# Kernel optimization log

Hardware: AMD Instinct MI355X
Metric: run time of the kernel (lower is better)

The kernel has to match this reference:

```python
import jax, jax.numpy as jnp
import numpy as np

HEADS, DIM, N = 16, 128, 2048
NEG = -1e9


def setup_inputs() -> dict:
    key = jax.random.key(0)
    ks = jax.random.split(key, 8)
    xavier = lambda k, shape, fan: jax.random.uniform(
        k, shape, jnp.float32, -1.0, 1.0) * np.sqrt(6.0 / fan)
    return {
        "q": jax.random.normal(ks[0], (N, DIM), jnp.float32),
        "k": jax.random.normal(ks[1], (N, DIM), jnp.float32),
        "v": jax.random.normal(ks[2], (N, DIM), jnp.float32),
        "mask": jax.random.randint(ks[3], (N, N), 0, 2) > 0,
        "Q": xavier(ks[4], (HEADS, DIM, DIM), 2 * DIM),
        "K": xavier(ks[5], (HEADS, DIM, DIM), 2 * DIM),
        "V": xavier(ks[6], (HEADS, DIM, DIM), 2 * DIM),
        "last": xavier(ks[7], (HEADS * DIM, DIM), HEADS * DIM + DIM),
    }


def reference(q, k, v, Q, K, V, last, mask):
    # per-head projections: [n, d] x [h, d, d] -> [h, n, d]
    qp = jnp.einsum('nd,hde->hne', q, Q)
    kp = jnp.einsum('nd,hde->hne', k, K)
    vp = jnp.einsum('nd,hde->hne', v, V)
    n = qp.shape[1]
    # NOTE: original computes k @ q^T and scales by sqrt(seq_len) (q.size(1) after projection)
    att = jnp.einsum('hid,hjd->hij', kp, qp)  # [h, n, n]
    fmask = mask.astype(jnp.float32)
    att = att * fmask / jnp.sqrt(jnp.float32(n)) + NEG * (1.0 - fmask)
    att = jax.nn.softmax(att, axis=2)
    out = jnp.einsum('hij,hjd->hid', att, vp)            # [h, n, d]
    out = jnp.transpose(out, (1, 0, 2)).reshape(n, -1)   # n (heads d)
    return out @ last
```

## Files before the change

### kernel.cpp

```cpp
#include <hip/hip_runtime.h>
#include <hip/hip_bf16.h>


#define HN 16
#define NN 2048
#define DD 128

typedef __attribute__((ext_vector_type(8))) short short8;
typedef __attribute__((ext_vector_type(4))) short short4v;
typedef __attribute__((ext_vector_type(4))) float float4v;
typedef __attribute__((ext_vector_type(16))) float f32x16;
typedef __attribute__((ext_vector_type(4))) unsigned int uint4v;

#define CROW(r) ((((r) & 3)) + 8 * ((r) >> 2))

__device__ inline unsigned short f2bf(float f) {
    unsigned int u = __builtin_bit_cast(unsigned int, f);
    unsigned int r = (u + 0x7fffu + ((u >> 16) & 1u)) >> 16;
    return (unsigned short)r;
}

__device__ inline unsigned int cvtpk(float lo, float hi) {
    unsigned int w;
    asm("v_cvt_pk_bf16_f32 %0, %1, %2" : "=v"(w) : "v"(lo), "v"(hi));
    return w;
}

__device__ inline void plswap(unsigned int& x, unsigned int& y) {
#if __has_builtin(__builtin_amdgcn_permlane32_swap)
    typedef int int2v __attribute__((ext_vector_type(2)));
    int2v r = __builtin_amdgcn_permlane32_swap((int)x, (int)y, false, false);
    x = (unsigned int)r[0];
    y = (unsigned int)r[1];
#else
    const unsigned int sx = (unsigned int)__shfl_xor((int)x, 32);
    const unsigned int sy = (unsigned int)__shfl_xor((int)y, 32);
    const bool hiHalf = (threadIdx.x & 32) != 0;
    const unsigned int nx = hiHalf ? sy : x;
    const unsigned int ny = hiHalf ? y : sx;
    x = nx; y = ny;
#endif
}

__device__ inline void bar_lds() {
    asm volatile("s_waitcnt lgkmcnt(0)" ::: "memory");
    __builtin_amdgcn_sched_barrier(0);
    __builtin_amdgcn_s_barrier();
    __builtin_amdgcn_sched_barrier(0);
}

__device__ inline short8 ld_bf8(const float* __restrict__ p) {
    const float4v a = *(const float4v*)p;
    const float4v b = *(const float4v*)(p + 4);
    short8 r;
    r[0] = (short)f2bf(a[0]); r[1] = (short)f2bf(a[1]);
    r[2] = (short)f2bf(a[2]); r[3] = (short)f2bf(a[3]);
    r[4] = (short)f2bf(b[0]); r[5] = (short)f2bf(b[1]);
    r[6] = (short)f2bf(b[2]); r[7] = (short)f2bf(b[3]);
    return r;
}

__device__ inline short8 ld2x4(const unsigned short* p) {
    const short4v lo = *(const short4v*)p;
    const short4v hi = *(const short4v*)(p + 4);
    short8 r;
    r[0] = lo[0]; r[1] = lo[1]; r[2] = lo[2]; r[3] = lo[3];
    r[4] = hi[0]; r[5] = hi[1]; r[6] = hi[2]; r[7] = hi[3];
    return r;
}

__global__ void sentinel_kernel(float* out, int n) {
    int i = blockIdx.x * 256 + threadIdx.x;
    if (i < n) out[i] = 2.0f;
}

__global__ __launch_bounds__(256) void maskpack2_kernel(
    const int* __restrict__ mask,
    unsigned long long* __restrict__ mb,
    float* __restrict__ out, int out_n)
{
    const int wgrp = blockIdx.x * 4 + (threadIdx.x >> 6);
    const int lane = threadIdx.x & 63;
    const int word0 = wgrp * 4;
    const int i = word0 >> 5;
    const int w = word0 & 31;
    const int* row = mask + (size_t)i * NN + w * 64;
    unsigned long long b[4];
#pragma unroll
    for (int c = 0; c < 4; c++)
        b[c] = __ballot(row[c * 64 + lane] != 0);
    if (lane == 0) {
#pragma unroll
        for (int c = 0; c < 4; c++) mb[word0 + c] = b[c];
    }
    const int z = blockIdx.x * 256 + threadIdx.x;
    if (z < out_n) out[z] = 0.f;
}

__global__ __launch_bounds__(256) void wprep_kernel(
    const float* __restrict__ Qw,
    const float* __restrict__ Kw,
    const float* __restrict__ Vw,
    unsigned short* __restrict__ wsW)
{
    __shared__ __align__(16) unsigned short Wt[128 * 132];
    const int h = blockIdx.x, t = blockIdx.y;
    const float* W = ((t == 0) ? Qw : ((t == 1) ? Kw : Vw)) + h * DD * DD;
    unsigned short* o = wsW + ((size_t)t * HN + h) * DD * DD;
    const int tid = threadIdx.x;

    for (int idx2 = tid * 2; idx2 < DD * DD; idx2 += 512) {
        const int d = idx2 >> 7, e = idx2 & 127;
        const float2 w2 = *(const float2*)(W + idx2);
        Wt[(e + 0) * 132 + d] = f2bf(w2.x);
        Wt[(e + 1) * 132 + d] = f2bf(w2.y);
    }
    __syncthreads();
    for (int idx8 = tid * 8; idx8 < DD * DD; idx8 += 2048) {
        const int e = idx8 >> 7, d = idx8 & 127;
        *(short8*)(o + idx8) = ld2x4(&Wt[e * 132 + d]);
    }
}

__global__ __launch_bounds__(256) void proj3_kernel(
    const float* __restrict__ q,
    const float* __restrict__ k,
    const float* __restrict__ v,
    const unsigned short* __restrict__ wsW,
    unsigned short* __restrict__ ws)
{
    __shared__ __align__(16) unsigned short Wt[128 * 136];
    const int t = blockIdx.z, h = blockIdx.y, cb = blockIdx.x;
    const int tid = threadIdx.x;
    const float* in = (t == 0) ? q : ((t == 1) ? k : v);
    const unsigned short* WTg = wsW + ((size_t)t * HN + h) * DD * DD;
    unsigned short* out = ws + (size_t)t * (HN * NN * DD) + (size_t)h * (NN * DD);

#pragma unroll
    for (int it = 0; it < 8; it++) {
        const int idx8 = tid * 8 + it * 2048;
        const int row = idx8 >> 7, col = idx8 & 127;
        *(short8*)(&Wt[row * 136 + col]) = *(const short8*)(WTg + idx8);
    }
    __syncthreads();

    const int wave = tid >> 6, lane = tid & 63;
    const int quad = lane >> 4, l16 = lane & 15;

#pragma unroll 1
    for (int rt = 0; rt < 2; rt++) {
        const int row0 = cb * 128 + rt * 64 + wave * 16;

        float4v acc[8];
#pragma unroll
        for (int c = 0; c < 8; c++) acc[c] = {0.f, 0.f, 0.f, 0.f};

        if (t < 2) {
#pragma unroll
            for (int kk = 0; kk < 4; kk++) {
                const short8 a = ld_bf8(in + (size_t)(row0 + l16) * DD + kk * 32 + quad * 8);
#pragma unroll
                for (int c = 0; c < 8; c++) {
                    const short8 b = *(const short8*)(&Wt[(c * 16 + l16) * 136 + kk * 32 + quad * 8]);
                    acc[c] = __builtin_amdgcn_mfma_f32_16x16x32_bf16(a, b, acc[c], 0, 0, 0);
                }
            }
#pragma unroll
            for (int c = 0; c < 8; c++)
#pragma unroll
                for (int r = 0; r < 4; r++)
                    out[(size_t)(row0 + quad * 4 + r) * DD + c * 16 + l16] = f2bf(acc[c][r]);
        } else {
#pragma unroll
            for (int kk = 0; kk < 4; kk++) {
                const short8 bv = ld_bf8(in + (size_t)(row0 + l16) * DD + kk * 32 + quad * 8);
#pragma unroll
                for (int c = 0; c < 8; c++) {
                    const short8 aw = *(const short8*)(&Wt[(c * 16 + l16) * 136 + kk * 32 + quad * 8]);
                    acc[c] = __builtin_amdgcn_mfma_f32_16x16x32_bf16(aw, bv, acc[c], 0, 0, 0);
                }
            }
#pragma unroll
            for (int c = 0; c < 8; c++)
#pragma unroll
                for (int r = 0; r < 4; r++)
                    out[(size_t)(c * 16 + quad * 4 + r) * NN + row0 + l16] = f2bf(acc[c][r]);
        }
    }
}

__global__ __launch_bounds__(256, 2) void attn_kernel(
    unsigned short* __restrict__ ws,
    const unsigned long long* __restrict__ mb)
{
    __shared__ __align__(16) unsigned short qs[2][64 * 136];
    __shared__ __align__(16) unsigned short vpTile[2][128 * 72];

    const int h = blockIdx.y, ib = blockIdx.x;
    const int tid = threadIdx.x;
    const int wave = tid >> 6, lane = tid & 63;
    const int ig = wave >> 1;
    const int h2 = wave & 1;
    const int l31 = lane & 31;
    const int hi = lane >> 5;

    const unsigned short* qp  = ws + (size_t)h * (NN * DD);
    const unsigned short* kp  = ws + (size_t)(HN * NN * DD) + (size_t)h * (NN * DD);
    const unsigned short* vpT = ws + (size_t)(2 * HN * NN * DD) + (size_t)h * (NN * DD);
    unsigned short* ao = ws + (size_t)(3 * HN * NN * DD);

    const int i0 = ib * 64;
    const float scale = 0.022097086912079612f;

    short8 kpf[8];
    {
        const int row = i0 + ig * 32 + l31;
#pragma unroll
        for (int kk = 0; kk < 8; kk++)
            kpf[kk] = *(const short8*)(kp + (size_t)row * DD + kk * 16 + hi * 8);
    }

    short8 rq[4], rv[4];

#define LOADT(J0) do {                                                         \
        _Pragma("unroll")                                                      \
        for (int it = 0; it < 4; it++) {                                       \
            const int idx = tid * 8 + it * 2048;                               \
            rq[it] = *(const short8*)(qp + (size_t)(J0) * DD + idx);           \
            rv[it] = *(const short8*)(vpT + (size_t)(idx >> 6) * NN + (J0) + (idx & 63)); \
        } } while (0)

#define WRITET(BUF) do {                                                       \
        _Pragma("unroll")                                                      \
        for (int it = 0; it < 4; it++) {                                       \
            const int idx = tid * 8 + it * 2048;                               \
            *(short8*)(&qs[BUF][(idx >> 7) * 136 + (idx & 127)]) = rq[it];     \
            *(short8*)(&vpTile[BUF][(idx >> 6) * 72 + (idx & 63)]) = rv[it];   \
        } } while (0)

    f32x16 o[4];
#pragma unroll
    for (int dt = 0; dt < 4; dt++)
#pragma unroll
        for (int r = 0; r < 16; r++) o[dt][r] = 0.f;
    float lacc = 0.f;

    auto COMPUTE = [&](int buf, int jt) {
        const unsigned long long mrow = mb[(size_t)(i0 + ig * 32 + l31) * 32 + jt];
        const unsigned int m2 = (unsigned int)(mrow >> (h2 * 32 + hi * 4));

        f32x16 s;
#pragma unroll
        for (int r = 0; r < 16; r++) s[r] = 0.f;
        __builtin_amdgcn_s_setprio(1);
#pragma unroll
        for (int kk = 0; kk < 8; kk++) {
            const short8 aq = *(const short8*)(&qs[buf][(h2 * 32 + l31) * 136 + kk * 16 + hi * 8]);
            s = __builtin_amdgcn_mfma_f32_32x32x16_bf16(aq, kpf[kk], s, 0, 0, 0);
        }
        __builtin_amdgcn_s_setprio(0);

#pragma unroll
        for (int r = 0; r < 16; r++) {
            const float x = ((m2 >> CROW(r)) & 1u) ? fmaf(s[r], scale, -5.0f) : -50.0f;
            s[r] = __expf(x);
        }
        float ls = (((s[0] + s[1]) + (s[2] + s[3])) + ((s[4] + s[5]) + (s[6] + s[7])))
                 + (((s[8] + s[9]) + (s[10] + s[11])) + ((s[12] + s[13]) + (s[14] + s[15])));
        ls += __shfl_xor(ls, 32);
        lacc += ls;

        short8 pa[2];
#pragma unroll
        for (int ks = 0; ks < 2; ks++) {
            const int b = ks * 8;
            unsigned int x0 = cvtpk(s[b + 0], s[b + 1]);
            unsigned int y0 = cvtpk(s[b + 4], s[b + 5]);
            unsigned int x1 = cvtpk(s[b + 2], s[b + 3]);
            unsigned int y1 = cvtpk(s[b + 6], s[b + 7]);
            plswap(x0, y0);
            plswap(x1, y1);
            uint4v w; w[0] = x0; w[1] = x1; w[2] = y0; w[3] = y1;
            pa[ks] = __builtin_bit_cast(short8, w);
        }

        __builtin_amdgcn_s_setprio(1);
#pragma unroll
        for (int ks = 0; ks < 2; ks++) {
#pragma unroll
            for (int dt = 0; dt < 4; dt++) {
                const short8 bv = *(const short8*)(&vpTile[buf][(dt * 32 + l31) * 72 + h2 * 32 + ks * 16 + hi * 8]);
                o[dt] = __builtin_amdgcn_mfma_f32_32x32x16_bf16(pa[ks], bv, o[dt], 0, 0, 0);
            }
        }
        __builtin_amdgcn_s_setprio(0);
    };

    LOADT(0);
    WRITET(0);
    LOADT(64);
    __syncthreads();

    int cur = 0;

#pragma unroll 1
    for (int jt = 0; jt < 30; ++jt) {
        WRITET(cur ^ 1);
        LOADT((jt + 2) * 64);
        COMPUTE(cur, jt);
        bar_lds();
        cur ^= 1;
    }
    WRITET(cur ^ 1);
    COMPUTE(cur, 30);
    bar_lds();
    cur ^= 1;
    COMPUTE(cur, 31);

#undef LOADT
#undef WRITET

    __syncthreads();
    float* obuf = (float*)&qs[0][0];
    float* lbuf = (float*)&vpTile[0][0];

    if (h2 == 1) {
#pragma unroll
        for (int dt = 0; dt < 4; dt++)
#pragma unroll
            for (int r = 0; r < 16; r++)
                obuf[(((ig * 2 + hi) * 4 + dt) * 16 + r) * 32 + l31] = o[dt][r];
        if (hi == 0) lbuf[ig * 32 + l31] = lacc;
    }
    __syncthreads();
    if (h2 == 0) {
        const float lt = lacc + lbuf[ig * 32 + l31];
        const float inv = (lt > 0.f) ? (1.0f / lt) : 0.f;
        if (hi == 0) lbuf[64 + ig * 32 + l31] = inv;
#pragma unroll
        for (int dt = 0; dt < 4; dt++)
#pragma unroll
            for (int r = 0; r < 16; r++) {
                const int row = CROW(r) + hi * 4;
                const float val = (o[dt][r] + obuf[(((ig * 2 + hi) * 4 + dt) * 16 + r) * 32 + l31])
                                  * lbuf[64 + ig * 32 + row];
                ao[(size_t)(i0 + ig * 32 + row) * (HN * DD) + h * DD + dt * 32 + l31] = f2bf(val);
            }
    }
}

__global__ __launch_bounds__(256) void final2_kernel(
    const unsigned short* __restrict__ ao,
    const float* __restrict__ last,
    float* __restrict__ outp)
{
    __shared__ __align__(16) unsigned short lt[32 * 516];
    const int tid = threadIdx.x;
    const int wave = tid >> 6, lane = tid & 63;
    const int quad = lane >> 4, l16 = lane & 15;
    const int i0 = blockIdx.x * 64;
    const int e0 = blockIdx.y * 32;
    const int k0 = blockIdx.z * 512;

#pragma unroll
    for (int idx2 = tid * 2; idx2 < 512 * 32; idx2 += 512) {
        const int kk = idx2 >> 5, e = idx2 & 31;
        const float2 w2 = *(const float2*)(last + (size_t)(k0 + kk) * DD + e0 + e);
        lt[(e + 0) * 516 + kk] = f2bf(w2.x);
        lt[(e + 1) * 516 + kk] = f2bf(w2.y);
    }
    __syncthreads();

    float4v acc[2];
    acc[0] = {0.f, 0.f, 0.f, 0.f};
    acc[1] = {0.f, 0.f, 0.f, 0.f};

    const unsigned short* arow = ao + (size_t)(i0 + wave * 16 + l16) * (HN * DD) + k0;

#pragma unroll
    for (int kb = 0; kb < 8; kb++) {
#pragma unroll
        for (int ks = 0; ks < 2; ks++) {
            const short8 a = *(const short8*)(arow + kb * 64 + ks * 32 + quad * 8);
#pragma unroll
            for (int dc = 0; dc < 2; dc++) {
                const short8 b = ld2x4(&lt[(dc * 16 + l16) * 516 + kb * 64 + ks * 32 + quad * 8]);
                acc[dc] = __builtin_amdgcn_mfma_f32_16x16x32_bf16(a, b, acc[dc], 0, 0, 0);
            }
        }
    }

#pragma unroll
    for (int r = 0; r < 4; r++)
#pragma unroll
        for (int dc = 0; dc < 2; dc++)
            atomicAdd(&outp[(size_t)(i0 + wave * 16 + quad * 4 + r) * DD + e0 + dc * 16 + l16],
                      acc[dc][r]);
}

extern "C" void kernel_launch(void* const* d_in, const int* in_sizes, int n_in,
                              void* d_out, int out_size, void* d_ws, size_t ws_size,
                              hipStream_t stream)
{
    const float* q    = (const float*)d_in[0];
    const float* k    = (const float*)d_in[1];
    const float* v    = (const float*)d_in[2];
    const int*   mask = (const int*)d_in[3];
    const float* Qw   = (const float*)d_in[4];
    const float* Kw   = (const float*)d_in[5];
    const float* Vw   = (const float*)d_in[6];
    const float* last = (const float*)d_in[7];
    unsigned short* ws  = (unsigned short*)d_ws;
    float* out = (float*)d_out;

    const size_t shorts_main = (size_t)4 * HN * NN * DD;
    const size_t mb_bytes = (size_t)NN * (NN / 64) * 8;
    const size_t needed = shorts_main * sizeof(unsigned short) + mb_bytes;
    if (ws_size < needed) {
        sentinel_kernel<<<(out_size + 255) / 256, 256, 0, stream>>>(out, out_size);
        return;
    }
    unsigned long long* mb = (unsigned long long*)(ws + shorts_main);
    unsigned short* wsW = ws + (size_t)3 * HN * NN * DD;

    maskpack2_kernel<<<dim3(NN * (NN / 64) / 16), 256, 0, stream>>>(mask, mb, out, out_size);
    wprep_kernel<<<dim3(16, 3), 256, 0, stream>>>(Qw, Kw, Vw, wsW);
    proj3_kernel<<<dim3(16, 16, 3), 256, 0, stream>>>(q, k, v, wsW, ws);
    attn_kernel<<<dim3(32, 16), 256, 0, stream>>>(ws, mb);
    final2_kernel<<<dim3(32, 4, 4), 256, 0, stream>>>(ws + (size_t)3 * HN * NN * DD, last, out);
}
```

Measured before the change: 161.6 us.

## Pre-swizzle Q/V projections into MFMA fragment layout and load directly to registers

The projection kernel now writes Q and V projections in a tiled layout that matches the MFMA operand fragments, and the mask bits are stored transposed so each tile reads contiguous words. The attention kernel drops the LDS double-buffered staging and barriers, loading Q and V fragments straight from global memory into registers with a two-stage register ping-pong. This removes LDS write/read traffic and per-tile block barriers, but raises register pressure and relies on L2/global latency being hidden by the prefetch of the next tile.

```diff
diff --git a/kernel.cpp b/kernel.cpp
--- a/kernel.cpp
+++ b/kernel.cpp
@@ -42,13 +42,6 @@
 #endif
 }
 
-__device__ inline void bar_lds() {
-    asm volatile("s_waitcnt lgkmcnt(0)" ::: "memory");
-    __builtin_amdgcn_sched_barrier(0);
-    __builtin_amdgcn_s_barrier();
-    __builtin_amdgcn_sched_barrier(0);
-}
-
 __device__ inline short8 ld_bf8(const float* __restrict__ p) {
     const float4v a = *(const float4v*)p;
     const float4v b = *(const float4v*)(p + 4);
@@ -76,7 +69,7 @@
 
 __global__ __launch_bounds__(256) void maskpack2_kernel(
     const int* __restrict__ mask,
-    unsigned long long* __restrict__ mb,
+    unsigned long long* __restrict__ mbT,
     float* __restrict__ out, int out_n)
 {
     const int wgrp = blockIdx.x * 4 + (threadIdx.x >> 6);
@@ -91,7 +84,7 @@
         b[c] = __ballot(row[c * 64 + lane] != 0);
     if (lane == 0) {
 #pragma unroll
-        for (int c = 0; c < 4; c++) mb[word0 + c] = b[c];
+        for (int c = 0; c < 4; c++) mbT[(size_t)(w + c) * NN + i] = b[c];
     }
     const int z = blockIdx.x * 256 + threadIdx.x;
     if (z < out_n) out[z] = 0.f;
@@ -122,7 +115,7 @@
     }
 }
 
-__global__ __launch_bounds__(256) void proj3_kernel(
+__global__ __launch_bounds__(256) void proj4_kernel(
     const float* __restrict__ q,
     const float* __restrict__ k,
     const float* __restrict__ v,
@@ -165,11 +158,22 @@
                     acc[c] = __builtin_amdgcn_mfma_f32_16x16x32_bf16(a, b, acc[c], 0, 0, 0);
                 }
             }
-#pragma unroll
-            for (int c = 0; c < 8; c++)
-#pragma unroll
-                for (int r = 0; r < 4; r++)
-                    out[(size_t)(row0 + quad * 4 + r) * DD + c * 16 + l16] = f2bf(acc[c][r]);
+            if (t == 0) {
+#pragma unroll
+                for (int c = 0; c < 8; c++)
+#pragma unroll
+                    for (int r = 0; r < 4; r++) {
+                        const int row = row0 + quad * 4 + r;
+                        out[(size_t)(((row >> 5) * 8 + c)) * 512 + (row & 31) * 16 + l16]
+                            = f2bf(acc[c][r]);
+                    }
+            } else {
+#pragma unroll
+                for (int c = 0; c < 8; c++)
+#pragma unroll
+                    for (int r = 0; r < 4; r++)
+                        out[(size_t)(row0 + quad * 4 + r) * DD + c * 16 + l16] = f2bf(acc[c][r]);
+            }
         } else {
 #pragma unroll
             for (int kk = 0; kk < 4; kk++) {
@@ -183,18 +187,20 @@
 #pragma unroll
             for (int c = 0; c < 8; c++)
 #pragma unroll
-                for (int r = 0; r < 4; r++)
-                    out[(size_t)(c * 16 + quad * 4 + r) * NN + row0 + l16] = f2bf(acc[c][r]);
+                for (int r = 0; r < 4; r++) {
+                    const int d = c * 16 + quad * 4 + r;
+                    out[(size_t)(row0 >> 4) * 2048 + d * 16 + l16] = f2bf(acc[c][r]);
+                }
         }
     }
 }
 
 __global__ __launch_bounds__(256, 2) void attn_kernel(
     unsigned short* __restrict__ ws,
-    const unsigned long long* __restrict__ mb)
-{
-    __shared__ __align__(16) unsigned short qs[2][64 * 136];
-    __shared__ __align__(16) unsigned short vpTile[2][128 * 72];
+    const unsigned long long* __restrict__ mbT)
+{
+    __shared__ __align__(16) float obuf[8192];
+    __shared__ float lbuf[192];
 
     const int h = blockIdx.y, ib = blockIdx.x;
     const int tid = threadIdx.x;
@@ -204,9 +210,9 @@
     const int l31 = lane & 31;
     const int hi = lane >> 5;
 
-    const unsigned short* qp  = ws + (size_t)h * (NN * DD);
+    const unsigned short* qA  = ws + (size_t)h * (NN * DD);
     const unsigned short* kp  = ws + (size_t)(HN * NN * DD) + (size_t)h * (NN * DD);
-    const unsigned short* vpT = ws + (size_t)(2 * HN * NN * DD) + (size_t)h * (NN * DD);
+    const unsigned short* vpB = ws + (size_t)(2 * HN * NN * DD) + (size_t)h * (NN * DD);
     unsigned short* ao = ws + (size_t)(3 * HN * NN * DD);
 
     const int i0 = ib * 64;
@@ -220,23 +226,8 @@
             kpf[kk] = *(const short8*)(kp + (size_t)row * DD + kk * 16 + hi * 8);
     }
 
-    short8 rq[4], rv[4];
-
-#define LOADT(J0) do {                                                         \
-        _Pragma("unroll")                                                      \
-        for (int it = 0; it < 4; it++) {                                       \
-            const int idx = tid * 8 + it * 2048;                               \
-            rq[it] = *(const short8*)(qp + (size_t)(J0) * DD + idx);           \
-            rv[it] = *(const short8*)(vpT + (size_t)(idx >> 6) * NN + (J0) + (idx & 63)); \
-        } } while (0)
-
-#define WRITET(BUF) do {                                                       \
-        _Pragma("unroll")                                                      \
-        for (int it = 0; it < 4; it++) {                                       \
-            const int idx = tid * 8 + it * 2048;                               \
-            *(short8*)(&qs[BUF][(idx >> 7) * 136 + (idx & 127)]) = rq[it];     \
-            *(short8*)(&vpTile[BUF][(idx >> 6) * 72 + (idx & 63)]) = rv[it];   \
-        } } while (0)
+    const unsigned short* qbase = qA + l31 * 16 + hi * 8;
+    const unsigned short* vbase = vpB + l31 * 16 + hi * 8;
 
     f32x16 o[4];
 #pragma unroll
@@ -245,8 +236,24 @@
         for (int r = 0; r < 16; r++) o[dt][r] = 0.f;
     float lacc = 0.f;
 
-    auto COMPUTE = [&](int buf, int jt) {
-        const unsigned long long mrow = mb[(size_t)(i0 + ig * 32 + l31) * 32 + jt];
+    short8 qfA[8], qfB[8];
+
+#define QLD(QF, JT) do {                                                        \
+        const unsigned short* p_ = qbase + (size_t)(((JT) * 2 + h2) * 8) * 512; \
+        _Pragma("unroll")                                                       \
+        for (int kk = 0; kk < 8; kk++)                                          \
+            QF[kk] = *(const short8*)(p_ + kk * 512);                           \
+    } while (0)
+
+    auto COMPUTE = [&](const short8 (&qf)[8], int jt) {
+        short8 vf[8];
+#pragma unroll
+        for (int ks = 0; ks < 2; ks++)
+#pragma unroll
+            for (int dt = 0; dt < 4; dt++)
+                vf[ks * 4 + dt] = *(const short8*)(vbase
+                    + (size_t)(jt * 4 + h2 * 2 + ks) * 2048 + dt * 512);
+        const unsigned long long mrow = mbT[(size_t)jt * NN + i0 + ig * 32 + l31];
         const unsigned int m2 = (unsigned int)(mrow >> (h2 * 32 + hi * 4));
 
         f32x16 s;
@@ -254,10 +261,8 @@
         for (int r = 0; r < 16; r++) s[r] = 0.f;
         __builtin_amdgcn_s_setprio(1);
 #pragma unroll
-        for (int kk = 0; kk < 8; kk++) {
-            const short8 aq = *(const short8*)(&qs[buf][(h2 * 32 + l31) * 136 + kk * 16 + hi * 8]);
-            s = __builtin_amdgcn_mfma_f32_32x32x16_bf16(aq, kpf[kk], s, 0, 0, 0);
-        }
+        for (int kk = 0; kk < 8; kk++)
+            s = __builtin_amdgcn_mfma_f32_32x32x16_bf16(qf[kk], kpf[kk], s, 0, 0, 0);
         __builtin_amdgcn_s_setprio(0);
 
 #pragma unroll
@@ -286,43 +291,22 @@
 
         __builtin_amdgcn_s_setprio(1);
 #pragma unroll
-        for (int ks = 0; ks < 2; ks++) {
-#pragma unroll
-            for (int dt = 0; dt < 4; dt++) {
-                const short8 bv = *(const short8*)(&vpTile[buf][(dt * 32 + l31) * 72 + h2 * 32 + ks * 16 + hi * 8]);
-                o[dt] = __builtin_amdgcn_mfma_f32_32x32x16_bf16(pa[ks], bv, o[dt], 0, 0, 0);
-            }
-        }
+        for (int ks = 0; ks < 2; ks++)
+#pragma unroll
+            for (int dt = 0; dt < 4; dt++)
+                o[dt] = __builtin_amdgcn_mfma_f32_32x32x16_bf16(pa[ks], vf[ks * 4 + dt], o[dt], 0, 0, 0);
         __builtin_amdgcn_s_setprio(0);
     };
 
-    LOADT(0);
-    WRITET(0);
-    LOADT(64);
-    __syncthreads();
-
-    int cur = 0;
-
+    QLD(qfA, 0);
 #pragma unroll 1
-    for (int jt = 0; jt < 30; ++jt) {
-        WRITET(cur ^ 1);
-        LOADT((jt + 2) * 64);
-        COMPUTE(cur, jt);
-        bar_lds();
-        cur ^= 1;
-    }
-    WRITET(cur ^ 1);
-    COMPUTE(cur, 30);
-    bar_lds();
-    cur ^= 1;
-    COMPUTE(cur, 31);
-
-#undef LOADT
-#undef WRITET
-
-    __syncthreads();
-    float* obuf = (float*)&qs[0][0];
-    float* lbuf = (float*)&vpTile[0][0];
+    for (int jt = 0; jt < 32; jt += 2) {
+        QLD(qfB, jt + 1);
+        COMPUTE(qfA, jt);
+        if (jt + 2 < 32) QLD(qfA, jt + 2);
+        COMPUTE(qfB, jt + 1);
+    }
+#undef QLD
 
     if (h2 == 1) {
 #pragma unroll
@@ -420,12 +404,12 @@
         sentinel_kernel<<<(out_size + 255) / 256, 256, 0, stream>>>(out, out_size);
         return;
     }
-    unsigned long long* mb = (unsigned long long*)(ws + shorts_main);
+    unsigned long long* mbT = (unsigned long long*)(ws + shorts_main);
     unsigned short* wsW = ws + (size_t)3 * HN * NN * DD;
 
-    maskpack2_kernel<<<dim3(NN * (NN / 64) / 16), 256, 0, stream>>>(mask, mb, out, out_size);
+    maskpack2_kernel<<<dim3(NN * (NN / 64) / 16), 256, 0, stream>>>(mask, mbT, out, out_size);
     wprep_kernel<<<dim3(16, 3), 256, 0, stream>>>(Qw, Kw, Vw, wsW);
-    proj3_kernel<<<dim3(16, 16, 3), 256, 0, stream>>>(q, k, v, wsW, ws);
-    attn_kernel<<<dim3(32, 16), 256, 0, stream>>>(ws, mb);
+    proj4_kernel<<<dim3(16, 16, 3), 256, 0, stream>>>(q, k, v, wsW, ws);
+    attn_kernel<<<dim3(32, 16), 256, 0, stream>>>(ws, mbT);
     final2_kernel<<<dim3(32, 4, 4), 256, 0, stream>>>(ws + (size_t)3 * HN * NN * DD, last, out);
 }
```

After: 160.5 us. Within noise of the previous version (-0.7%).
